# Kernel tuning notes

Hardware: AMD Instinct MI355X
Metric: run time of the kernel (lower is better)

The kernel has to match this reference:

```python
import jax, jax.numpy as jnp
import numpy as np

NUM_HEADS = 12
EPS = 1e-5


def _pool_norm(t, w, g, b, thw, stride):
    # t: [B, heads, 1+L, hd]. Depthwise Conv3d pooling on non-cls tokens, then LayerNorm(hd).
    B, Hn, _, hd = t.shape
    cls, body = t[:, :, :1], t[:, :, 1:]
    T, Hs, Ws = thw
    x = body.reshape(B * Hn, T, Hs, Ws, hd).transpose(0, 4, 1, 2, 3)  # [B*heads, hd, T, H, W]
    pad = [(w.shape[2] // 2,) * 2, (w.shape[3] // 2,) * 2, (w.shape[4] // 2,) * 2]
    y = jax.lax.conv_general_dilated(x, w, window_strides=stride, padding=pad,
                                     feature_group_count=hd,
                                     dimension_numbers=('NCDHW', 'OIDHW', 'NCDHW'))
    Tp, Hp, Wp = y.shape[2], y.shape[3], y.shape[4]
    y = y.reshape(B, Hn, hd, Tp * Hp * Wp).transpose(0, 1, 3, 2)  # [B, heads, Lp, hd]
    y = jnp.concatenate([cls, y], axis=2)
    mu = y.mean(-1, keepdims=True)
    var = ((y - mu) ** 2).mean(-1, keepdims=True)
    return (y - mu) * jax.lax.rsqrt(var + EPS) * g + b


def _forward(x, Wq, Wk, Wv, Wproj, b_proj, pq, pk, pv, gq, bq, gk, bk, gv, bv, thw):
    B, N, C = x.shape
    hd = C // NUM_HEADS
    def proj(W):
        return (x @ W.T).reshape(B, N, NUM_HEADS, hd).transpose(0, 2, 1, 3)  # [B, heads, N, hd]
    q = _pool_norm(proj(Wq), pq, gq, bq, thw, (1, 2, 2))
    k = _pool_norm(proj(Wk), pk, gk, bk, thw, (1, 4, 4))
    v = _pool_norm(proj(Wv), pv, gv, bv, thw, (1, 4, 4))
    scale = hd ** -0.5
    attn = jax.nn.softmax(jnp.einsum('bhqd,bhkd->bhqk', q * scale, k), axis=-1)
    o = jnp.einsum('bhqk,bhkd->bhqd', attn, v)
    o = o.transpose(0, 2, 1, 3).reshape(B, o.shape[2], C)
    return o @ Wproj.T + b_proj


def setup_inputs() -> dict:
    key = jax.random.key(0)
    ks = jax.random.split(key, 8)
    B, T, H, W, C = 8, 8, 28, 28, 768
    hd = C // NUM_HEADS
    N = T * H * W + 1  # cls token
    s = lambda k, sh: jax.random.normal(k, sh, jnp.float32) * 0.02
    return {
        'x': jax.random.normal(ks[0], (B, N, C), jnp.float32),
        'Wq': s(ks[1], (C, C)), 'Wk': s(ks[2], (C, C)), 'Wv': s(ks[3], (C, C)),
        'Wproj': s(ks[4], (C, C)), 'b_proj': jnp.zeros((C,), jnp.float32),
        'pool_q_w': s(ks[5], (hd, 1, 3, 3, 3)),
        'pool_k_w': s(ks[6], (hd, 1, 3, 3, 3)),
        'pool_v_w': s(ks[7], (hd, 1, 3, 3, 3)),
        'gq': jnp.ones((hd,), jnp.float32), 'bq': jnp.zeros((hd,), jnp.float32),
        'gk': jnp.ones((hd,), jnp.float32), 'bk': jnp.zeros((hd,), jnp.float32),
        'gv': jnp.ones((hd,), jnp.float32), 'bv': jnp.zeros((hd,), jnp.float32),
        'thw_t': 8, 'thw_h': 28, 'thw_w': 28,
    }


def reference(x, Wq, Wk, Wv, Wproj, b_proj, pool_q_w, pool_k_w, pool_v_w,
              gq, bq, gk, bk, gv, bv, thw_t, thw_h, thw_w):
    return _forward(x, Wq, Wk, Wv, Wproj, b_proj, pool_q_w, pool_k_w, pool_v_w,
                    gq, bq, gk, bk, gv, bv, (thw_t, thw_h, thw_w))
```

## Files before the change

### kernel.cpp

```cpp
#include <hip/hip_runtime.h>

using bf16   = __bf16;
using bf16x4 = __attribute__((ext_vector_type(4))) __bf16;
using bf16x8 = __attribute__((ext_vector_type(8))) __bf16;
using f32x4  = __attribute__((ext_vector_type(4))) float;
using u32x4  = __attribute__((ext_vector_type(4))) unsigned int;

#define MFMA16(a,b,c) __builtin_amdgcn_mfma_f32_16x16x32_bf16((a),(b),(c),0,0,0)

__device__ inline void glds16(const void* g, void* l) {
    __builtin_amdgcn_global_load_lds(
        (__attribute__((address_space(1))) void*)(const_cast<void*>(g)),
        (__attribute__((address_space(3))) void*)(l), 16, 0, 0);
}

constexpr int CB   = 8;
constexpr int NH   = 12;
constexpr int CC   = 768;
constexpr int HD   = 64;
constexpr int TT   = 8, HH = 28, WW = 28;
constexpr int NTOK = TT*HH*WW + 1;
constexpr int MX   = CB*NTOK;
constexpr int MXP  = 50304;
constexpr int NQ   = 1569, NQP = 1600;
constexpr int NK   = 393,  NKP = 416;
constexpr int MO   = CB*NQ;
constexpr int MOP  = 12672;
constexpr int CTOK = 1 + TT*20*20;
constexpr int MKV  = CB*CTOK;
constexpr int MKVP = 25856;

__global__ __launch_bounds__(256) void cast_f32_bf16(const float* __restrict__ src,
                                                     bf16* __restrict__ dst,
                                                     int nvalid, int ntotal) {
    int i = (blockIdx.x * 256 + threadIdx.x) * 4;
    int stride = gridDim.x * 256 * 4;
    for (; i < ntotal; i += stride) {
        bf16x4 o;
        if (i + 3 < nvalid) {
            f32x4 v = *(const f32x4*)(src + i);
            #pragma unroll
            for (int e = 0; e < 4; ++e) o[e] = (bf16)v[e];
        } else {
            #pragma unroll
            for (int e = 0; e < 4; ++e) {
                int k = i + e;
                o[e] = (bf16)((k < nvalid) ? src[k] : 0.f);
            }
        }
        *(bf16x4*)(dst + i) = o;
    }
}

__global__ __launch_bounds__(256) void transpose_w3(const float* __restrict__ w0,
                                                    const float* __restrict__ w1,
                                                    const float* __restrict__ w2,
                                                    float* __restrict__ wt) {
    int i = blockIdx.x * 256 + threadIdx.x;
    if (i >= 3 * 1728) return;
    int setn = i / 1728, j = i % 1728;
    const float* src = (setn == 0) ? w0 : (setn == 1) ? w1 : w2;
    int tap = j / 64, c = j % 64;
    wt[i] = src[c * 27 + tap];
}

__global__ void bound_kernel(const float* __restrict__ gq, const float* __restrict__ bq,
                             const float* __restrict__ gk, const float* __restrict__ bk,
                             float* __restrict__ out) {
    const int c = threadIdx.x;
    float mgq = fabsf(gq[c]), sbq = bq[c] * bq[c];
    float mgk = fabsf(gk[c]), sbk = bk[c] * bk[c];
    #pragma unroll
    for (int m = 1; m < 64; m <<= 1) {
        mgq = fmaxf(mgq, __shfl_xor(mgq, m)); sbq += __shfl_xor(sbq, m);
        mgk = fmaxf(mgk, __shfl_xor(mgk, m)); sbk += __shfl_xor(sbk, m);
    }
    if (c == 0) {
        const float Bq = 8.f * mgq + sqrtf(sbq);
        const float Bk = 8.f * mgk + sqrtf(sbk);
        out[0] = 0.125f * Bq * Bk;
    }
}

__global__ __launch_bounds__(512, 2) void gemmU(const bf16* __restrict__ xb,
                                                const bf16* __restrict__ wqkv,
                                                bf16* __restrict__ tmpq,
                                                bf16* __restrict__ tmpkv) {
    extern __shared__ char lds[];
    const int nwg = gridDim.x;
    const int xcd = blockIdx.x & 7, loc = blockIdx.x >> 3;
    const int q8 = nwg >> 3, r8 = nwg & 7;
    const int wgid = (xcd < r8 ? xcd * (q8 + 1) : r8 * (q8 + 1) + (xcd - r8) * q8) + loc;

    const int tid = threadIdx.x, lane = tid & 63, w = tid >> 6;
    const int li = lane & 15, lg = lane >> 4;
    const int wr = w >> 2, wc = w & 3;
    const int lr  = lane >> 3;
    const int lsw = ((lane & 7) ^ lr) << 3;

    const bool isQ = wgid < 591;
    int bm, bn, Mv, ldc;
    const bf16* Bb;
    bf16* C;
    if (isQ) { bm = wgid / 3;        bn = wgid % 3;        Mv = MXP;  ldc = 768;
               Bb = wqkv + (size_t)bn * 256 * 768;               C = tmpq; }
    else     { int t = wgid - 591;   bm = t / 6; bn = t % 6; Mv = MKVP; ldc = 1536;
               Bb = wqkv + (size_t)(768 + bn * 256) * 768;       C = tmpkv; }

    const bf16* abase[4];
    const bf16* bbase[4];
    #pragma unroll
    for (int h_ = 0; h_ < 4; ++h_) {
        int gr = bm * 256 + h_ * 64 + w * 8 + lr;
        size_t orig;
        if (isQ) {
            if (gr > MXP - 1) gr = MXP - 1;
            orig = (size_t)gr;
        } else {
            if (gr > MKV - 1) gr = MKV - 1;
            const unsigned b = (unsigned)gr / 3201u;
            const unsigned p = (unsigned)gr % 3201u;
            if (p == 0) orig = (size_t)b * NTOK;
            else {
                const unsigned q  = p - 1;
                const unsigned t2 = q / 400u, rem = q % 400u;
                const unsigned hi = rem / 20u, wi = rem % 20u;
                const int ih = 4 * (int)((hi + 1) / 3) + (int)((hi + 1) % 3) - 1;
                const int iw = 4 * (int)((wi + 1) / 3) + (int)((wi + 1) % 3) - 1;
                orig = (size_t)b * NTOK + 1 + ((size_t)t2 * HH + ih) * WW + iw;
            }
        }
        abase[h_] = xb + orig * 768 + lsw;
        bbase[h_] = Bb + (size_t)(h_ * 64 + w * 8 + lr) * 768 + lsw;
    }

    const int sw_  = (li & 7) << 4;
    const int swc0 = (lg * 16) ^ sw_;
    const int swc1 = (64 | (lg * 16)) ^ sw_;

#define STAGE_T(Tt, buf) do {                                                        \
        char* d_ = lds + (buf) * 65536;                                              \
        _Pragma("unroll")                                                            \
        for (int h_ = 0; h_ < 4; ++h_)                                               \
            glds16(abase[h_] + (Tt) * 64, d_ + (h_ * 64 + w * 8) * 128);             \
        _Pragma("unroll")                                                            \
        for (int h_ = 0; h_ < 4; ++h_)                                               \
            glds16(bbase[h_] + (Tt) * 64, d_ + 32768 + (h_ * 64 + w * 8) * 128);     \
    } while (0)

    f32x4 acc[8][4] = {};
    bf16x8 aF[8], bF[4];

#define READ_K(sw)                                                                   \
    _Pragma("unroll") for (int mf = 0; mf < 8; ++mf)                                 \
        aF[mf] = *(const bf16x8*)(bufA + (size_t)(wr * 128 + mf * 16 + li) * 128 + (sw)); \
    _Pragma("unroll") for (int nf = 0; nf < 4; ++nf)                                 \
        bF[nf] = *(const bf16x8*)(bufB + (size_t)(wc * 64 + nf * 16 + li) * 128 + (sw));

#define MFMA_K()                                                                     \
    _Pragma("unroll") for (int mf = 0; mf < 8; ++mf)                                 \
    _Pragma("unroll") for (int nf = 0; nf < 4; ++nf)                                 \
        acc[mf][nf] = MFMA16(aF[mf], bF[nf], acc[mf][nf]);

    STAGE_T(0, 0);
    STAGE_T(1, 1);
    asm volatile("s_waitcnt vmcnt(8)" ::: "memory");
    __builtin_amdgcn_s_barrier();
    __builtin_amdgcn_sched_barrier(0);

    #pragma unroll
    for (int T = 0; T < 12; ++T) {
        const char* bufA = lds + (T & 1) * 65536;
        const char* bufB = bufA + 32768;
        if (T >= 1 && T < 11) STAGE_T(T + 1, (T + 1) & 1);
        READ_K(swc0);
        __builtin_amdgcn_s_setprio(1);
        MFMA_K();
        __builtin_amdgcn_s_setprio(0);
        READ_K(swc1);
        __builtin_amdgcn_s_setprio(1);
        MFMA_K();
        __builtin_amdgcn_s_setprio(0);
        asm volatile("s_waitcnt lgkmcnt(0)" ::: "memory");
        if (T < 11) asm volatile("s_waitcnt vmcnt(0)" ::: "memory");
        __builtin_amdgcn_s_barrier();
        __builtin_amdgcn_sched_barrier(0);
    }
#undef STAGE_T
#undef READ_K
#undef MFMA_K

    #pragma unroll
    for (int mf = 0; mf < 8; ++mf) {
        const int row0 = bm * 256 + wr * 128 + mf * 16 + lg * 4;
        #pragma unroll
        for (int nf = 0; nf < 4; ++nf) {
            const int col = bn * 256 + wc * 64 + nf * 16 + li;
            #pragma unroll
            for (int r = 0; r < 4; ++r) {
                const int row = row0 + r;
                if (row < Mv)
                    C[(size_t)row * ldc + col] = (bf16)acc[mf][nf][r];
            }
        }
    }
}

__global__ __launch_bounds__(512, 2) void gemmF(const bf16* __restrict__ A,
                                                const bf16* __restrict__ Bw,
                                                float* __restrict__ Cptr,
                                                const float* __restrict__ bias,
                                                int nbn, int Mvalid, int Aclamp) {
    extern __shared__ char lds[];
    const int nwg = gridDim.x;
    const int xcd = blockIdx.x & 7, loc = blockIdx.x >> 3;
    const int q8 = nwg >> 3, r8 = nwg & 7;
    const int wgid = (xcd < r8 ? xcd * (q8 + 1) : r8 * (q8 + 1) + (xcd - r8) * q8) + loc;
    const int bm = wgid / nbn, bn = wgid % nbn;

    const int tid = threadIdx.x, lane = tid & 63, w = tid >> 6;
    const int li = lane & 15, lg = lane >> 4;
    const int wr = w >> 2, wc = w & 3;
    const int lr  = lane >> 3;
    const int lsw = ((lane & 7) ^ lr) << 3;
    const bf16* Agp = A  + (size_t)bm * 256 * 768;
    const bf16* Bgp = Bw + (size_t)bn * 256 * 768;
    const int clampA = Aclamp - bm * 256;

    const int sw_  = (li & 7) << 4;
    const int swc0 = (lg * 16) ^ sw_;
    const int swc1 = (64 | (lg * 16)) ^ sw_;

#define STAGE_T(Tt, buf) do {                                                        \
        char* d_ = lds + (buf) * 65536;                                              \
        _Pragma("unroll")                                                            \
        for (int h_ = 0; h_ < 4; ++h_) {                                             \
            const int r0_ = h_ * 64 + w * 8;                                         \
            int gr_ = r0_ + lr; if (gr_ >= clampA) gr_ = clampA - 1;                 \
            glds16(Agp + (size_t)gr_ * 768 + (Tt) * 64 + lsw, d_ + r0_ * 128);       \
        }                                                                            \
        _Pragma("unroll")                                                            \
        for (int h_ = 0; h_ < 4; ++h_) {                                             \
            const int r0_ = h_ * 64 + w * 8;                                         \
            glds16(Bgp + (size_t)(r0_ + lr) * 768 + (Tt) * 64 + lsw,                 \
                   d_ + 32768 + r0_ * 128);                                          \
        } } while (0)

    f32x4 acc[8][4] = {};
    bf16x8 aF[8], bF[4];

#define READ_K(sw)                                                                   \
    _Pragma("unroll") for (int mf = 0; mf < 8; ++mf)                                 \
        aF[mf] = *(const bf16x8*)(bufA + (size_t)(wr * 128 + mf * 16 + li) * 128 + (sw)); \
    _Pragma("unroll") for (int nf = 0; nf < 4; ++nf)                                 \
        bF[nf] = *(const bf16x8*)(bufB + (size_t)(wc * 64 + nf * 16 + li) * 128 + (sw));

#define MFMA_K()                                                                     \
    _Pragma("unroll") for (int mf = 0; mf < 8; ++mf)                                 \
    _Pragma("unroll") for (int nf = 0; nf < 4; ++nf)                                 \
        acc[mf][nf] = MFMA16(aF[mf], bF[nf], acc[mf][nf]);

    STAGE_T(0, 0);
    STAGE_T(1, 1);
    asm volatile("s_waitcnt vmcnt(8)" ::: "memory");
    __builtin_amdgcn_s_barrier();
    __builtin_amdgcn_sched_barrier(0);

    #pragma unroll
    for (int T = 0; T < 12; ++T) {
        const char* bufA = lds + (T & 1) * 65536;
        const char* bufB = bufA + 32768;
        if (T >= 1 && T < 11) STAGE_T(T + 1, (T + 1) & 1);
        READ_K(swc0);
        __builtin_amdgcn_s_setprio(1);
        MFMA_K();
        __builtin_amdgcn_s_setprio(0);
        READ_K(swc1);
        __builtin_amdgcn_s_setprio(1);
        MFMA_K();
        __builtin_amdgcn_s_setprio(0);
        asm volatile("s_waitcnt lgkmcnt(0)" ::: "memory");
        if (T < 11) asm volatile("s_waitcnt vmcnt(0)" ::: "memory");
        __builtin_amdgcn_s_barrier();
        __builtin_amdgcn_sched_barrier(0);
    }
#undef STAGE_T
#undef READ_K
#undef MFMA_K

    #pragma unroll
    for (int mf = 0; mf < 8; ++mf) {
        const int row0 = bm * 256 + wr * 128 + mf * 16 + lg * 4;
        #pragma unroll
        for (int nf = 0; nf < 4; ++nf) {
            const int col = bn * 256 + wc * 64 + nf * 16 + li;
            #pragma unroll
            for (int r = 0; r < 4; ++r) {
                const int row = row0 + r;
                if (row < Mvalid)
                    Cptr[(size_t)row * 768 + col] = acc[mf][nf][r] + bias[col];
            }
        }
    }
}

template<int S, int OH, int OW, int CH, int NP, int NPpad, int SRCSTRIDE, bool COMPACT>
__global__ __launch_bounds__(256) void pool_norm2(const bf16* __restrict__ P,
                                                  const float* __restrict__ wt,
                                                  const float* __restrict__ gamma,
                                                  const float* __restrict__ beta,
                                                  bf16* __restrict__ outp,
                                                  float outScale) {
    constexpr int TASKS = TT * OH * CH + 1;
    const int w = threadIdx.x >> 6, lane = threadIdx.x & 63;
    const int gw = blockIdx.x * 4 + w;
    const int bh = gw / TASKS, task = gw % TASKS;
    const int b = bh / NH, head = bh % NH;
    const int owg = lane >> 3, cg = lane & 7, c = cg * 8;
    const size_t rowbase = COMPACT ? (size_t)b * CTOK : (size_t)b * NTOK;
    const size_t pbase = rowbase * SRCSTRIDE + head * HD + c;

    if (task == TASKS - 1) {
        if (owg == 0) {
            bf16x8 v = *(const bf16x8*)(P + pbase);
            float a[8];
            #pragma unroll
            for (int e = 0; e < 8; ++e) a[e] = (float)v[e];
            float s = 0;
            #pragma unroll
            for (int e = 0; e < 8; ++e) s += a[e];
            s += __shfl_xor(s, 1); s += __shfl_xor(s, 2); s += __shfl_xor(s, 4);
            const float mu = s * 0.015625f;
            float v2 = 0;
            #pragma unroll
            for (int e = 0; e < 8; ++e) { float d = a[e] - mu; v2 += d * d; }
            v2 += __shfl_xor(v2, 1); v2 += __shfl_xor(v2, 2); v2 += __shfl_xor(v2, 4);
            const float rs = rsqrtf(v2 * 0.015625f + 1e-5f);
            f32x4 g0 = *(const f32x4*)(gamma + c), g1 = *(const f32x4*)(gamma + c + 4);
            f32x4 b0 = *(const f32x4*)(beta + c),  b1 = *(const f32x4*)(beta + c + 4);
            bf16x8 o;
            #pragma unroll
            for (int e = 0; e < 4; ++e) {
                o[e]     = (bf16)(((a[e]     - mu) * rs * g0[e] + b0[e]) * outScale);
                o[4 + e] = (bf16)(((a[4 + e] - mu) * rs * g1[e] + b1[e]) * outScale);
            }
            *(bf16x8*)(outp + ((size_t)bh * NPpad) * HD + c) = o;
        } else {
            bf16x8 z = {};
            for (int p = NP + owg - 1; p < NPpad; p += 7)
                *(bf16x8*)(outp + ((size_t)bh * NPpad + p) * HD + c) = z;
        }
        return;
    }

    const int t  = task / (OH * CH);
    const int r2 = task % (OH * CH);
    const int oh = r2 / CH;
    const int ow = (r2 % CH) * 8 + owg;
    const bool active = (ow < OW);

    float acc[8] = {0, 0, 0, 0, 0, 0, 0, 0};
    #pragma unroll
    for (int dt = 0; dt < 3; ++dt) {
        const int it = t + dt - 1;
        if (it < 0 || it >= TT) continue;
        #pragma unroll
        for (int dh = 0; dh < 3; ++dh) {
            int rowh;
            if constexpr (COMPACT) {
                const int hi = 3 * oh + dh - 1;
                if (hi < 0) continue;
                rowh = 1 + it * 400 + hi * 20;
            } else {
                const int ih = oh * S + dh - 1;
                if (ih < 0 || ih >= HH) continue;
                rowh = 1 + (it * HH + ih) * WW;
            }
            #pragma unroll
            for (int dw = 0; dw < 3; ++dw) {
                int rowoff;
                bool ok;
                if constexpr (COMPACT) {
                    const int wi = 3 * ow + dw - 1;
                    ok = active && (wi >= 0);
                    rowoff = rowh + wi;
                } else {
                    const int iw = ow * S + dw - 1;
                    ok = active && (iw >= 0);
                    rowoff = rowh + iw;
                }
                if (ok) {
                    bf16x8 v = *(const bf16x8*)(P + pbase + (size_t)rowoff * SRCSTRIDE);
                    const float* wp = wt + ((dt * 3 + dh) * 3 + dw) * 64 + c;
                    f32x4 w0 = *(const f32x4*)wp, w1 = *(const f32x4*)(wp + 4);
                    #pragma unroll
                    for (int e = 0; e < 4; ++e) {
                        acc[e]     += w0[e] * (float)v[e];
                        acc[4 + e] += w1[e] * (float)v[4 + e];
                    }
                }
            }
        }
    }
    float s = 0;
    #pragma unroll
    for (int e = 0; e < 8; ++e) s += acc[e];
    s += __shfl_xor(s, 1); s += __shfl_xor(s, 2); s += __shfl_xor(s, 4);
    const float mu = s * 0.015625f;
    float v2 = 0;
    #pragma unroll
    for (int e = 0; e < 8; ++e) { float d = acc[e] - mu; v2 += d * d; }
    v2 += __shfl_xor(v2, 1); v2 += __shfl_xor(v2, 2); v2 += __shfl_xor(v2, 4);
    const float rs = rsqrtf(v2 * 0.015625f + 1e-5f);
    if (active) {
        f32x4 g0 = *(const f32x4*)(gamma + c), g1 = *(const f32x4*)(gamma + c + 4);
        f32x4 b0 = *(const f32x4*)(beta + c),  b1 = *(const f32x4*)(beta + c + 4);
        bf16x8 o;
        #pragma unroll
        for (int e = 0; e < 4; ++e) {
            o[e]     = (bf16)(((acc[e]     - mu) * rs * g0[e] + b0[e]) * outScale);
            o[4 + e] = (bf16)(((acc[4 + e] - mu) * rs * g1[e] + b1[e]) * outScale);
        }
        const int p = 1 + (t * OH + oh) * OW + ow;
        *(bf16x8*)(outp + ((size_t)bh * NPpad + p) * HD + c) = o;
    }
}

__global__ __launch_bounds__(256) void attn_kernel(const bf16* __restrict__ qn,
                                                   const bf16* __restrict__ kn,
                                                   const bf16* __restrict__ vn,
                                                   bf16* __restrict__ ob,
                                                   const float* __restrict__ Mptr) {
    __shared__ bf16 Kl[2][32][72];
    __shared__ bf16 Vt[2][64][40];
    __shared__ bf16 Pl[4][16][40];

    const int tid = threadIdx.x, l = tid & 63, w = tid >> 6;
    const int li = l & 15, lg = l >> 4;
    const int bh = blockIdx.y;
    const int b = bh / NH, head = bh % NH;
    const int qbase = blockIdx.x * 64 + w * 16;
    const float M = Mptr[0];

    const bf16* qp = qn + ((size_t)bh * NQP + qbase + li) * HD + lg * 8;
    const bf16x8 aq0 = *(const bf16x8*)qp;
    const bf16x8 aq1 = *(const bf16x8*)(qp + 32);

    const int srow = tid >> 3, scol = (tid & 7) * 8;
    const int sj = tid & 31, sd8 = tid >> 5;
    const bf16* kbase = kn + (size_t)bh * NKP * HD;
    const bf16* vbase = vn + (size_t)bh * NKP * HD;

    u32x4 kv = *(const u32x4*)(kbase + srow * HD + scol);
    u32x4 vv = *(const u32x4*)(vbase + sj * HD + sd8 * 8);
    *(u32x4*)&Kl[0][srow][scol] = kv;
    {
        bf16x8 t = __builtin_bit_cast(bf16x8, vv);
        #pragma unroll
        for (int e = 0; e < 8; ++e) Vt[0][sd8 * 8 + e][sj] = t[e];
    }

    f32x4 oacc[4] = {};
    float lpart[4] = {0.f, 0.f, 0.f, 0.f};

    for (int kt = 0; kt < 13; ++kt) {
        const int cur = kt & 1;
        if (kt < 12) {
            kv = *(const u32x4*)(kbase + (kt + 1) * 32 * HD + srow * HD + scol);
            vv = *(const u32x4*)(vbase + (kt + 1) * 32 * HD + sj * HD + sd8 * 8);
        }
        __syncthreads();

        f32x4 c0 = {}, c1 = {};
        const bf16x8 b00 = *(const bf16x8*)&Kl[cur][li][lg * 8];
        const bf16x8 b01 = *(const bf16x8*)&Kl[cur][li][32 + lg * 8];
        const bf16x8 b10 = *(const bf16x8*)&Kl[cur][16 + li][lg * 8];
        const bf16x8 b11 = *(const bf16x8*)&Kl[cur][16 + li][32 + lg * 8];
        __builtin_amdgcn_s_setprio(1);
        c0 = MFMA16(aq0, b00, c0); c0 = MFMA16(aq1, b01, c0);
        c1 = MFMA16(aq0, b10, c1); c1 = MFMA16(aq1, b11, c1);
        __builtin_amdgcn_s_setprio(0);

        float p0[4], p1[4];
        #pragma unroll
        for (int r = 0; r < 4; ++r) {
            p0[r] = __expf(c0[r] - M);
            p1[r] = __expf(c1[r] - M);
        }
        if (kt == 12) {
            const bool m0 = (384 + li) >= NK;
            #pragma unroll
            for (int r = 0; r < 4; ++r) { if (m0) p0[r] = 0.f; p1[r] = 0.f; }
        }
        #pragma unroll
        for (int r = 0; r < 4; ++r) {
            lpart[r] += p0[r] + p1[r];
            Pl[w][lg * 4 + r][li]      = (bf16)p0[r];
            Pl[w][lg * 4 + r][16 + li] = (bf16)p1[r];
        }
        const bf16x8 ap = *(const bf16x8*)&Pl[w][li][lg * 8];
        __builtin_amdgcn_s_setprio(1);
        #pragma unroll
        for (int dg = 0; dg < 4; ++dg) {
            const bf16x8 bv = *(const bf16x8*)&Vt[cur][dg * 16 + li][lg * 8];
            oacc[dg] = MFMA16(ap, bv, oacc[dg]);
        }
        __builtin_amdgcn_s_setprio(0);

        if (kt < 12) {
            const int nxt = cur ^ 1;
            *(u32x4*)&Kl[nxt][srow][scol] = kv;
            bf16x8 t = __builtin_bit_cast(bf16x8, vv);
            #pragma unroll
            for (int e = 0; e < 8; ++e) Vt[nxt][sd8 * 8 + e][sj] = t[e];
        }
    }
    #pragma unroll
    for (int r = 0; r < 4; ++r) {
        float lsum = lpart[r];
        lsum += __shfl_xor(lsum, 1);
        lsum += __shfl_xor(lsum, 2);
        lsum += __shfl_xor(lsum, 4);
        lsum += __shfl_xor(lsum, 8);
        const int q = qbase + lg * 4 + r;
        if (q < NQ) {
            const float inv = 1.f / lsum;
            const size_t off = ((size_t)(b * NQ + q)) * CC + head * HD;
            #pragma unroll
            for (int dg = 0; dg < 4; ++dg)
                ob[off + dg * 16 + li] = (bf16)(oacc[dg][r] * inv);
        }
    }
}

extern "C" void kernel_launch(void* const* d_in, const int* in_sizes, int n_in,
                              void* d_out, int out_size, void* d_ws, size_t ws_size,
                              hipStream_t stream) {
    const float* x     = (const float*)d_in[0];
    const float* Wq    = (const float*)d_in[1];
    const float* Wk    = (const float*)d_in[2];
    const float* Wv    = (const float*)d_in[3];
    const float* Wproj = (const float*)d_in[4];
    const float* bproj = (const float*)d_in[5];
    const float* pqw   = (const float*)d_in[6];
    const float* pkw   = (const float*)d_in[7];
    const float* pvw   = (const float*)d_in[8];
    const float* gq    = (const float*)d_in[9];
    const float* bq    = (const float*)d_in[10];
    const float* gk    = (const float*)d_in[11];
    const float* bk    = (const float*)d_in[12];
    const float* gv    = (const float*)d_in[13];
    const float* bv    = (const float*)d_in[14];

    if (ws_size < 364000000ULL) return;
    char* ws = (char*)d_ws;
    bf16* xb    = (bf16*)(ws);
    bf16* wqkv  = (bf16*)(ws + 77266944);
    bf16* wpb   = (bf16*)(ws + 80805888);
    bf16* tmpq  = (bf16*)(ws + 81985536);
    bf16* tmpkv = (bf16*)(ws + 159252480);
    bf16* qn    = (bf16*)(ws + 238682112);
    bf16* kn    = (bf16*)(ws + 258342912);
    bf16* vnb   = (bf16*)(ws + 263454720);
    bf16* ob    = (bf16*)(ws + 268566528);
    float* wt   = (float*)(ws + 288030720);
    float* Mb   = (float*)(ws + 288051456);

    const int WSZ = 589824;

    (void)hipFuncSetAttribute((const void*)gemmU,
                              hipFuncAttributeMaxDynamicSharedMemorySize, 131072);
    (void)hipFuncSetAttribute((const void*)gemmF,
                              hipFuncAttributeMaxDynamicSharedMemorySize, 131072);

    transpose_w3<<<21, 256, 0, stream>>>(pqw, pkw, pvw, wt);
    bound_kernel<<<1, 64, 0, stream>>>(gq, bq, gk, bk, Mb);
    cast_f32_bf16<<<4096, 256, 0, stream>>>(x, xb, MX * CC, MXP * CC);
    cast_f32_bf16<<<576, 256, 0, stream>>>(Wq, wqkv,            WSZ, WSZ);
    cast_f32_bf16<<<576, 256, 0, stream>>>(Wk, wqkv + WSZ,      WSZ, WSZ);
    cast_f32_bf16<<<576, 256, 0, stream>>>(Wv, wqkv + 2 * WSZ,  WSZ, WSZ);
    cast_f32_bf16<<<576, 256, 0, stream>>>(Wproj, wpb,          WSZ, WSZ);

    gemmU<<<1197, 512, 131072, stream>>>(xb, wqkv, tmpq, tmpkv);

    pool_norm2<2, 14, 14, 2, NQ, NQP, 768,  false><<<5400, 256, 0, stream>>>(tmpq,        wt,        gq, bq, qn,  0.125f);
    pool_norm2<4, 7, 7, 1, NK, NKP, 1536, true ><<<1368, 256, 0, stream>>>(tmpkv,       wt + 1728, gk, bk, kn,  1.0f);
    pool_norm2<4, 7, 7, 1, NK, NKP, 1536, true ><<<1368, 256, 0, stream>>>(tmpkv + 768, wt + 3456, gv, bv, vnb, 1.0f);

    attn_kernel<<<dim3(25, 96), 256, 0, stream>>>(qn, kn, vnb, ob, Mb);

    gemmF<<<50 * 3, 512, 131072, stream>>>(ob, wpb, (float*)d_out, bproj, 3, MO, MOP);
}
```

Before: 360.2 us.

## Narrow gemmF N-tile, fuse weight casts, XCD-remap pool and attention grids

The output projection GEMM now uses 256x128 tiles instead of 256x256. That doubles the grid from 150 to 300 workgroups, which fills more CUs, and cuts LDS per block. The four weight cast launches are merged into one kernel that writes the contiguous wqkv/wpb buffer. The pool_norm and attention kernels now remap block IDs across the XCDs for better L2 locality, with attention moved to a 1D grid. The narrower tile lowers per-block arithmetic intensity and reloads the A tile more often.

```diff
diff --git a/kernel.cpp b/kernel.cpp
--- a/kernel.cpp
+++ b/kernel.cpp
@@ -12,6 +12,12 @@
     __builtin_amdgcn_global_load_lds(
         (__attribute__((address_space(1))) void*)(const_cast<void*>(g)),
         (__attribute__((address_space(3))) void*)(l), 16, 0, 0);
+}
+
+__device__ inline int xcd_remap(int bid, int nwg) {
+    const int xcd = bid & 7, loc = bid >> 3;
+    const int q8 = nwg >> 3, r8 = nwg & 7;
+    return (xcd < r8 ? xcd * (q8 + 1) : r8 * (q8 + 1) + (xcd - r8) * q8) + loc;
 }
 
 constexpr int CB   = 8;
@@ -52,6 +58,23 @@
     }
 }
 
+__global__ __launch_bounds__(256) void cast_w4(const float* __restrict__ w0,
+                                               const float* __restrict__ w1,
+                                               const float* __restrict__ w2,
+                                               const float* __restrict__ w3,
+                                               bf16* __restrict__ dst) {
+    constexpr int WSZ = 589824;
+    int i = (blockIdx.x * 256 + threadIdx.x) * 4;
+    if (i >= 4 * WSZ) return;
+    const int setn = i / WSZ, j = i % WSZ;
+    const float* src = (setn == 0) ? w0 : (setn == 1) ? w1 : (setn == 2) ? w2 : w3;
+    f32x4 v = *(const f32x4*)(src + j);
+    bf16x4 o;
+    #pragma unroll
+    for (int e = 0; e < 4; ++e) o[e] = (bf16)v[e];
+    *(bf16x4*)(dst + i) = o;
+}
+
 __global__ __launch_bounds__(256) void transpose_w3(const float* __restrict__ w0,
                                                     const float* __restrict__ w1,
                                                     const float* __restrict__ w2,
@@ -87,10 +110,7 @@
                                                 bf16* __restrict__ tmpq,
                                                 bf16* __restrict__ tmpkv) {
     extern __shared__ char lds[];
-    const int nwg = gridDim.x;
-    const int xcd = blockIdx.x & 7, loc = blockIdx.x >> 3;
-    const int q8 = nwg >> 3, r8 = nwg & 7;
-    const int wgid = (xcd < r8 ? xcd * (q8 + 1) : r8 * (q8 + 1) + (xcd - r8) * q8) + loc;
+    const int wgid = xcd_remap(blockIdx.x, gridDim.x);
 
     const int tid = threadIdx.x, lane = tid & 63, w = tid >> 6;
     const int li = lane & 15, lg = lane >> 4;
@@ -212,10 +232,7 @@
                                                 const float* __restrict__ bias,
                                                 int nbn, int Mvalid, int Aclamp) {
     extern __shared__ char lds[];
-    const int nwg = gridDim.x;
-    const int xcd = blockIdx.x & 7, loc = blockIdx.x >> 3;
-    const int q8 = nwg >> 3, r8 = nwg & 7;
-    const int wgid = (xcd < r8 ? xcd * (q8 + 1) : r8 * (q8 + 1) + (xcd - r8) * q8) + loc;
+    const int wgid = xcd_remap(blockIdx.x, gridDim.x);
     const int bm = wgid / nbn, bn = wgid % nbn;
 
     const int tid = threadIdx.x, lane = tid & 63, w = tid >> 6;
@@ -224,7 +241,7 @@
     const int lr  = lane >> 3;
     const int lsw = ((lane & 7) ^ lr) << 3;
     const bf16* Agp = A  + (size_t)bm * 256 * 768;
-    const bf16* Bgp = Bw + (size_t)bn * 256 * 768;
+    const bf16* Bgp = Bw + (size_t)bn * 128 * 768;
     const int clampA = Aclamp - bm * 256;
 
     const int sw_  = (li & 7) << 4;
@@ -232,7 +249,7 @@
     const int swc1 = (64 | (lg * 16)) ^ sw_;
 
 #define STAGE_T(Tt, buf) do {                                                        \
-        char* d_ = lds + (buf) * 65536;                                              \
+        char* d_ = lds + (buf) * 49152;                                              \
         _Pragma("unroll")                                                            \
         for (int h_ = 0; h_ < 4; ++h_) {                                             \
             const int r0_ = h_ * 64 + w * 8;                                         \
@@ -240,35 +257,35 @@
             glds16(Agp + (size_t)gr_ * 768 + (Tt) * 64 + lsw, d_ + r0_ * 128);       \
         }                                                                            \
         _Pragma("unroll")                                                            \
-        for (int h_ = 0; h_ < 4; ++h_) {                                             \
+        for (int h_ = 0; h_ < 2; ++h_) {                                             \
             const int r0_ = h_ * 64 + w * 8;                                         \
             glds16(Bgp + (size_t)(r0_ + lr) * 768 + (Tt) * 64 + lsw,                 \
                    d_ + 32768 + r0_ * 128);                                          \
         } } while (0)
 
-    f32x4 acc[8][4] = {};
-    bf16x8 aF[8], bF[4];
+    f32x4 acc[8][2] = {};
+    bf16x8 aF[8], bF[2];
 
 #define READ_K(sw)                                                                   \
     _Pragma("unroll") for (int mf = 0; mf < 8; ++mf)                                 \
         aF[mf] = *(const bf16x8*)(bufA + (size_t)(wr * 128 + mf * 16 + li) * 128 + (sw)); \
-    _Pragma("unroll") for (int nf = 0; nf < 4; ++nf)                                 \
-        bF[nf] = *(const bf16x8*)(bufB + (size_t)(wc * 64 + nf * 16 + li) * 128 + (sw));
+    _Pragma("unroll") for (int nf = 0; nf < 2; ++nf)                                 \
+        bF[nf] = *(const bf16x8*)(bufB + (size_t)(wc * 32 + nf * 16 + li) * 128 + (sw));
 
 #define MFMA_K()                                                                     \
     _Pragma("unroll") for (int mf = 0; mf < 8; ++mf)                                 \
-    _Pragma("unroll") for (int nf = 0; nf < 4; ++nf)                                 \
+    _Pragma("unroll") for (int nf = 0; nf < 2; ++nf)                                 \
         acc[mf][nf] = MFMA16(aF[mf], bF[nf], acc[mf][nf]);
 
     STAGE_T(0, 0);
     STAGE_T(1, 1);
-    asm volatile("s_waitcnt vmcnt(8)" ::: "memory");
+    asm volatile("s_waitcnt vmcnt(6)" ::: "memory");
     __builtin_amdgcn_s_barrier();
     __builtin_amdgcn_sched_barrier(0);
 
     #pragma unroll
     for (int T = 0; T < 12; ++T) {
-        const char* bufA = lds + (T & 1) * 65536;
+        const char* bufA = lds + (T & 1) * 49152;
         const char* bufB = bufA + 32768;
         if (T >= 1 && T < 11) STAGE_T(T + 1, (T + 1) & 1);
         READ_K(swc0);
@@ -292,8 +309,8 @@
     for (int mf = 0; mf < 8; ++mf) {
         const int row0 = bm * 256 + wr * 128 + mf * 16 + lg * 4;
         #pragma unroll
-        for (int nf = 0; nf < 4; ++nf) {
-            const int col = bn * 256 + wc * 64 + nf * 16 + li;
+        for (int nf = 0; nf < 2; ++nf) {
+            const int col = bn * 128 + wc * 32 + nf * 16 + li;
             #pragma unroll
             for (int r = 0; r < 4; ++r) {
                 const int row = row0 + r;
@@ -313,7 +330,7 @@
                                                   float outScale) {
     constexpr int TASKS = TT * OH * CH + 1;
     const int w = threadIdx.x >> 6, lane = threadIdx.x & 63;
-    const int gw = blockIdx.x * 4 + w;
+    const int gw = xcd_remap(blockIdx.x, gridDim.x) * 4 + w;
     const int bh = gw / TASKS, task = gw % TASKS;
     const int b = bh / NH, head = bh % NH;
     const int owg = lane >> 3, cg = lane & 7, c = cg * 8;
@@ -437,9 +454,10 @@
 
     const int tid = threadIdx.x, l = tid & 63, w = tid >> 6;
     const int li = l & 15, lg = l >> 4;
-    const int bh = blockIdx.y;
+    const int wgid = xcd_remap(blockIdx.x, gridDim.x);
+    const int bh = wgid / 25;
     const int b = bh / NH, head = bh % NH;
-    const int qbase = blockIdx.x * 64 + w * 16;
+    const int qbase = (wgid % 25) * 64 + w * 16;
     const float M = Mptr[0];
 
     const bf16* qp = qn + ((size_t)bh * NQP + qbase + li) * HD + lg * 8;
@@ -566,20 +584,15 @@
     float* wt   = (float*)(ws + 288030720);
     float* Mb   = (float*)(ws + 288051456);
 
-    const int WSZ = 589824;
-
     (void)hipFuncSetAttribute((const void*)gemmU,
                               hipFuncAttributeMaxDynamicSharedMemorySize, 131072);
     (void)hipFuncSetAttribute((const void*)gemmF,
-                              hipFuncAttributeMaxDynamicSharedMemorySize, 131072);
+                              hipFuncAttributeMaxDynamicSharedMemorySize, 98304);
 
     transpose_w3<<<21, 256, 0, stream>>>(pqw, pkw, pvw, wt);
     bound_kernel<<<1, 64, 0, stream>>>(gq, bq, gk, bk, Mb);
     cast_f32_bf16<<<4096, 256, 0, stream>>>(x, xb, MX * CC, MXP * CC);
-    cast_f32_bf16<<<576, 256, 0, stream>>>(Wq, wqkv,            WSZ, WSZ);
-    cast_f32_bf16<<<576, 256, 0, stream>>>(Wk, wqkv + WSZ,      WSZ, WSZ);
-    cast_f32_bf16<<<576, 256, 0, stream>>>(Wv, wqkv + 2 * WSZ,  WSZ, WSZ);
-    cast_f32_bf16<<<576, 256, 0, stream>>>(Wproj, wpb,          WSZ, WSZ);
+    cast_w4<<<2304, 256, 0, stream>>>(Wq, Wk, Wv, Wproj, wqkv);
 
     gemmU<<<1197, 512, 131072, stream>>>(xb, wqkv, tmpq, tmpkv);
 
@@ -587,7 +600,7 @@
     pool_norm2<4, 7, 7, 1, NK, NKP, 1536, true ><<<1368, 256, 0, stream>>>(tmpkv,       wt + 1728, gk, bk, kn,  1.0f);
     pool_norm2<4, 7, 7, 1, NK, NKP, 1536, true ><<<1368, 256, 0, stream>>>(tmpkv + 768, wt + 3456, gv, bv, vnb, 1.0f);
 
-    attn_kernel<<<dim3(25, 96), 256, 0, stream>>>(qn, kn, vnb, ob, Mb);
-
-    gemmF<<<50 * 3, 512, 131072, stream>>>(ob, wpb, (float*)d_out, bproj, 3, MO, MOP);
-}
+    attn_kernel<<<2400, 256, 0, stream>>>(qn, kn, vnb, ob, Mb);
+
+    gemmF<<<50 * 6, 512, 98304, stream>>>(ob, wpb, (float*)d_out, bproj, 6, MO, MOP);
+}
```

Measured after the change: 352.9 us. -2.0%, faster.
